# Kernel optimization log

Hardware: AMD Instinct MI355X
Metric: run time of the kernel (lower is better)

Reference implementation:

```python
import jax, jax.numpy as jnp
import numpy as np

RF = 16       # receptive_field
STRIDE = 16   # sim_strides
ALPHA = 0.3   # tf.keras LeakyReLU default alpha
EPS = 1e-3    # tf.keras BatchNormalization default epsilon


def _leaky(x):
    return jnp.where(x > 0, x, ALPHA * x)


def _bn_train(x, gamma, beta):
    # training-mode batch norm over (B, H, W), channel-last
    mu = jnp.mean(x, axis=(0, 1, 2))
    var = jnp.var(x, axis=(0, 1, 2))
    return (x - mu) * jax.lax.rsqrt(var + EPS) * gamma + beta


def _cbl(x, W, gamma, beta):
    # 1x1 conv (== channel matmul) + BN + LeakyReLU
    y = jnp.einsum('bhwc,cd->bhwd', x, W)
    return _leaky(_bn_train(y, gamma, beta))


def setup_inputs() -> dict:
    key = jax.random.key(0)
    ks = jax.random.split(key, 4)
    B, H, Wd, C = 4, 64, 64, 256
    s = 1.0 / np.sqrt(C)
    return {
        'inputs': jax.random.normal(ks[0], (B, H, Wd, C), jnp.float32),
        'Wq': jax.random.normal(ks[1], (C, C), jnp.float32) * s,
        'gq': jnp.ones((C,), jnp.float32), 'bq': jnp.zeros((C,), jnp.float32),
        'Wk': jax.random.normal(ks[2], (C, C), jnp.float32) * s,
        'gk': jnp.ones((C,), jnp.float32), 'bk': jnp.zeros((C,), jnp.float32),
        'Wv': jax.random.normal(ks[3], (C, C), jnp.float32) * s,
        'gv': jnp.ones((C,), jnp.float32), 'bv': jnp.zeros((C,), jnp.float32),
        'g1': jnp.ones((C,), jnp.float32), 'b1': jnp.zeros((C,), jnp.float32),
    }


def _windows(x):
    # x: [B,H,W,C] -> [B, nH*nW, RF, RF, C] overlapping-capable window gather
    H, Wd = x.shape[1], x.shape[2]
    nH = (H - RF) // STRIDE + 1
    nW = (Wd - RF) // STRIDE + 1
    ih = (jnp.arange(nH) * STRIDE)[:, None] + jnp.arange(RF)[None, :]  # [nH,RF]
    iw = (jnp.arange(nW) * STRIDE)[:, None] + jnp.arange(RF)[None, :]  # [nW,RF]
    xw = x[:, ih][:, :, :, iw]            # [B,nH,RF,nW,RF,C]
    xw = xw.transpose(0, 1, 3, 2, 4, 5)   # [B,nH,nW,RF,RF,C]
    return xw.reshape(x.shape[0], nH * nW, RF, RF, x.shape[3])


def reference(inputs, Wq, gq, bq, Wk, gk, bk, Wv, gv, bv, g1, b1):
    Q = _cbl(inputs, Wq, gq, bq)   # [B,H,W,C]
    K = _cbl(inputs, Wk, gk, bk)
    V = _cbl(inputs, Wv, gv, bv)
    C = Q.shape[-1]
    Kw = _windows(K)               # [B,N,RF,RF,C]
    Vw = _windows(V)
    # full-Q x window-K attention, summed over windows (matches nested loop)
    scores = jnp.einsum('bijc,bnpqc->bnijpq', Q, Kw) / jnp.sqrt(jnp.asarray(C, Q.dtype))
    scores = _leaky(scores)
    yout = jnp.einsum('bnijpq,bnpqc->bijc', scores, Vw)  # sum over windows n
    y = _bn_train(yout, g1, b1)
    # softmax jointly over spatial axes (1,2)
    m = jnp.max(y, axis=(1, 2), keepdims=True)
    e = jnp.exp(y - m)
    return e / jnp.sum(e, axis=(1, 2), keepdims=True)
```

## Files before the change

### kernel.cpp

```cpp
#include <hip/hip_runtime.h>
#include <stdint.h>


typedef __attribute__((ext_vector_type(8)))  short short8;
typedef __attribute__((ext_vector_type(4)))  float f32x4;
typedef __attribute__((ext_vector_type(16))) float f32x16;
typedef __attribute__((ext_vector_type(4)))  unsigned short ushort4v;

#define ALPHA 0.3f
#define EPS   1e-3
#define NTOT  16384.0

__device__ __forceinline__ unsigned short f2bf(float f){
  unsigned u = __float_as_uint(f);
  u += 0x7FFFu + ((u>>16)&1u);
  return (unsigned short)(u>>16);
}
__device__ __forceinline__ float bf2f(unsigned short u){
  return __uint_as_float((unsigned)u << 16);
}
__device__ __forceinline__ float lrelu(float x){ return fmaxf(x, ALPHA*x); }

__global__ __launch_bounds__(256)
void k_prep(const float* __restrict__ X,
            const float* __restrict__ Wq,
            const float* __restrict__ Wk,
            const float* __restrict__ Wv,
            unsigned short* __restrict__ Xb,
            unsigned short* __restrict__ Wt,
            float* __restrict__ zws){
  int blk = blockIdx.x, tid = threadIdx.x;
  if (blk < 4096){
    int i = (blk*256 + tid)*4;
    float4 v = *(const float4*)(X + i);
    ushort4v o; o.x = f2bf(v.x); o.y = f2bf(v.y); o.z = f2bf(v.z); o.w = f2bf(v.w);
    *(ushort4v*)(Xb + i) = o;
  } else {
    int o = (blk - 4096)*256 + tid;
    int p = o >> 16, rem = o & 65535;
    int j = rem >> 8, c = rem & 255;
    const float* W = (p==0) ? Wq : ((p==1) ? Wk : Wv);
    Wt[o] = f2bf(W[c*256 + j]);
    if (o < 5120) zws[o] = 0.f;
  }
}

__global__ __launch_bounds__(256)
void k_qkv_gemm(const unsigned short* __restrict__ X,
                const unsigned short* __restrict__ Wt,
                unsigned short* __restrict__ YQK, unsigned short* __restrict__ Yv,
                double* __restrict__ st){
  __shared__ __align__(16) unsigned short At[64*264];
  __shared__ __align__(16) unsigned short Bt[64*264];
  int tid = threadIdx.x;
  int g = blockIdx.x;
  int xcd = g & 7, r = g >> 3;
  int nb = r % 12, mb = xcd*32 + r/12;
#pragma unroll
  for (int it = 0; it < 8; ++it){
    int s = it*256 + tid;
    int row = s >> 5, ch = s & 31;
    uint4 a = *(const uint4*)(X  + ((size_t)(mb*64 + row))*256 + ch*8);
    uint4 b = *(const uint4*)(Wt + ((size_t)(nb*64 + row))*256 + ch*8);
    *(uint4*)(At + row*264 + ch*8) = a;
    *(uint4*)(Bt + row*264 + ch*8) = b;
  }
  __syncthreads();
  int lane = tid & 63, wv = tid >> 6;
  int ln15 = lane & 15, quad = lane >> 4;
  int rw = (wv & 1)*32, cw = (wv >> 1)*32;
  f32x4 acc[2][2] = {};
#pragma unroll
  for (int ks = 0; ks < 8; ++ks){
    short8 afr[2], bfr[2];
#pragma unroll
    for (int mt = 0; mt < 2; ++mt){
      int rr = rw + mt*16 + ln15;
      afr[mt] = *(const short8*)(At + rr*264 + (ks*4+quad)*8);
    }
#pragma unroll
    for (int nt = 0; nt < 2; ++nt){
      int rr = cw + nt*16 + ln15;
      bfr[nt] = *(const short8*)(Bt + rr*264 + (ks*4+quad)*8);
    }
#pragma unroll
    for (int mt = 0; mt < 2; ++mt)
#pragma unroll
      for (int nt = 0; nt < 2; ++nt)
        acc[mt][nt] = __builtin_amdgcn_mfma_f32_16x16x32_bf16(afr[mt], bfr[nt], acc[mt][nt], 0,0,0);
  }
  float ps[2] = {0.f, 0.f}, pq[2] = {0.f, 0.f};
#pragma unroll
  for (int mt = 0; mt < 2; ++mt)
#pragma unroll
    for (int nt = 0; nt < 2; ++nt)
#pragma unroll
      for (int rr = 0; rr < 4; ++rr){
        float v = acc[mt][nt][rr];
        ps[nt] += v; pq[nt] += v*v;
      }
  if (nb < 8){
    int proj = nb >> 2;
    unsigned short* base = YQK + (size_t)proj*(16384*256);
    int l5c = ln15 >> 3, j = ln15 & 7;
#pragma unroll
    for (int mt = 0; mt < 2; ++mt){
      int gg = (mb*64 + rw + mt*16) >> 5;
      int l31r0 = ((rw + mt*16) & 31) + quad*4;
#pragma unroll
      for (int nt = 0; nt < 2; ++nt){
        int ks2 = ((nb & 3)*64 + cw + nt*16) >> 4;
#pragma unroll
        for (int rr = 0; rr < 4; ++rr){
          size_t chunk = (size_t)((gg*16 + ks2)*64 + l5c*32 + l31r0 + rr);
          base[chunk*8 + j] = f2bf(acc[mt][nt][rr]);
        }
      }
    }
  } else {
    int vc0 = (nb - 8)*64 + cw;
#pragma unroll
    for (int mt = 0; mt < 2; ++mt)
#pragma unroll
      for (int nt = 0; nt < 2; ++nt)
#pragma unroll
        for (int rr = 0; rr < 4; ++rr){
          int row = mb*64 + rw + mt*16 + quad*4 + rr;
          Yv[(size_t)row*256 + vc0 + nt*16 + ln15] = f2bf(acc[mt][nt][rr]);
        }
  }
  __syncthreads();
  float* red = (float*)At;
  if (tid < 128) red[tid] = 0.f;
  __syncthreads();
#pragma unroll
  for (int nt = 0; nt < 2; ++nt){
    int colL = cw + nt*16 + ln15;
    atomicAdd(&red[colL],      ps[nt]);
    atomicAdd(&red[64 + colL], pq[nt]);
  }
  __syncthreads();
  if (tid < 64){
    int cc = nb*64 + tid;
    atomicAdd(&st[cc],       (double)red[tid]);
    atomicAdd(&st[768 + cc], (double)red[64 + tid]);
  }
}

__global__ __launch_bounds__(256)
void k_bn(const unsigned short* __restrict__ YQK, const unsigned short* __restrict__ Yv,
          const double* __restrict__ st,
          const float* __restrict__ gq, const float* __restrict__ bq,
          const float* __restrict__ gk, const float* __restrict__ bk,
          const float* __restrict__ gv, const float* __restrict__ bv,
          unsigned short* __restrict__ Qf, unsigned short* __restrict__ Kf,
          unsigned short* __restrict__ Vf){
  __shared__ float sc_s[256], sh_s[256];
  __shared__ unsigned short tile[64][66];
  int tid = threadIdx.x;
  int blk = blockIdx.x;
  if (blk < 4096){
    int proj = blk >> 11;
    {
      int c = tid;
      int cc = proj*256 + c;
      double mu  = st[cc]     * (1.0/NTOT);
      double var = st[768+cc] * (1.0/NTOT) - mu*mu;
      double g = proj ? (double)gk[c] : (double)gq[c];
      double b = proj ? (double)bk[c] : (double)bq[c];
      double a = g / sqrt(var + EPS);
      float f = proj ? 1.f : 0.0625f;
      sc_s[c] = (float)a * f;
      sh_s[c] = (float)(b - mu*a) * f;
    }
    __syncthreads();
    int oc = blk*256 + tid;
    int rest = oc & 524287;
    int ks = (rest >> 6) & 15, l5c = (rest >> 5) & 1;
    int ch0 = ks*16 + l5c*8;
    uint4 yin = *(const uint4*)(YQK + (size_t)oc*8);
    const unsigned short* yp = (const unsigned short*)&yin;
    const float* sc = sc_s + ch0;
    const float* sh = sh_s + ch0;
    unsigned short rr[8];
#pragma unroll
    for (int e = 0; e < 8; ++e){
      float v = bf2f(yp[e]);
      rr[e] = f2bf(lrelu(v*sc[e] + sh[e]));
    }
    uint4 u;
    u.x = (unsigned)rr[0] | ((unsigned)rr[1]<<16);
    u.y = (unsigned)rr[2] | ((unsigned)rr[3]<<16);
    u.z = (unsigned)rr[4] | ((unsigned)rr[5]<<16);
    u.w = (unsigned)rr[6] | ((unsigned)rr[7]<<16);
    *(uint4*)((proj ? Kf : Qf) + (size_t)rest*8) = u;
  } else {
    int b2 = blk - 4096;
    int pt = b2 & 63, ct = (b2 >> 6) & 3, b = b2 >> 8;
    if (tid < 64){
      int c = ct*64 + tid;
      int cc = 512 + c;
      double mu  = st[cc]     * (1.0/NTOT);
      double var = st[768+cc] * (1.0/NTOT) - mu*mu;
      double a = (double)gv[c] / sqrt(var + EPS);
      sc_s[tid] = (float)a;
      sh_s[tid] = (float)((double)bv[c] - mu*a);
    }
    __syncthreads();
#pragma unroll
    for (int kpass = 0; kpass < 2; ++kpass){
      int idx = kpass*256 + tid;
      int px = idx >> 3, co = idx & 7;
      size_t t = (size_t)b*4096 + pt*64 + px;
      uint4 u = *(const uint4*)(Yv + t*256 + ct*64 + co*8);
      const unsigned short* up = (const unsigned short*)&u;
      int c0 = co*8;
#pragma unroll
      for (int e = 0; e < 8; ++e){
        float v = bf2f(up[e]);
        tile[px][c0+e] = f2bf(lrelu(v*sc_s[c0+e] + sh_s[c0+e]));
      }
    }
    __syncthreads();
#pragma unroll
    for (int it = 0; it < 2; ++it){
      int m = it*256 + tid;
      int c2 = m >> 3, kg = m & 7;
      int ch = ct*64 + c2;
      int gc = b*8 + (ch >> 5), l31c = ch & 31;
      int kp = pt*4 + (kg >> 1), l5k = kg & 1;
      unsigned short r0 = tile[kg*8+0][c2], r1 = tile[kg*8+1][c2];
      unsigned short r2 = tile[kg*8+2][c2], r3 = tile[kg*8+3][c2];
      unsigned short r4 = tile[kg*8+4][c2], r5 = tile[kg*8+5][c2];
      unsigned short r6 = tile[kg*8+6][c2], r7 = tile[kg*8+7][c2];
      uint4 u;
      u.x = (unsigned)r0 | ((unsigned)r1<<16);
      u.y = (unsigned)r2 | ((unsigned)r3<<16);
      u.z = (unsigned)r4 | ((unsigned)r5<<16);
      u.w = (unsigned)r6 | ((unsigned)r7<<16);
      *(uint4*)(Vf + ((size_t)((gc*256 + kp)*64 + l5k*32 + l31c))*8) = u;
    }
  }
}

__global__ __launch_bounds__(512, 4)
void k_attn(const unsigned short* __restrict__ Qf,
            const unsigned short* __restrict__ Kf,
            const unsigned short* __restrict__ Vf,
            float* __restrict__ P0, float* __restrict__ P1){
  __shared__ __align__(16) unsigned short Ql[64*256];
  __shared__ __align__(16) unsigned short Sl[64*264];
  int tid = threadIdx.x;
  int blk = blockIdx.x;
  int qt = blk >> 3, combo = blk & 7;
  int b = combo >> 1, half = combo & 1;
  int q0 = qt*64;
  int lane = tid & 63, w = tid >> 6;
  int l31 = lane & 31, l5 = lane >> 5;
  float* P = half ? P1 : P0;

  int gq0 = b*128 + qt*2;
  {
    const uint4* src = (const uint4*)(Qf + (size_t)gq0*8192);
    uint4* dst = (uint4*)Ql;
#pragma unroll
    for (int it = 0; it < 4; ++it) dst[it*512 + tid] = src[it*512 + tid];
  }
  __syncthreads();

  f32x16 acc2[2] = {};
  int gk0 = b*128 + half*64 + w;
  const unsigned short* kb = Kf + (size_t)gk0*8192 + lane*8;
  const unsigned short* vb = Vf + ((size_t)((b*8 + w)*256 + half*128))*512 + lane*8;
  const unsigned short* qa0 = Ql + lane*8;
  const unsigned short* qa1 = Ql + 16*512 + lane*8;

  for (int kt = 0; kt < 8; ++kt){
    f32x16 a1[2] = {};
    const unsigned short* kbt = kb + (size_t)kt*8*8192;
    __builtin_amdgcn_s_setprio(1);
#pragma unroll
    for (int ks = 0; ks < 16; ++ks){
      short8 kf = *(const short8*)(kbt + ks*512);
      short8 q0v = *(const short8*)(qa0 + ks*512);
      short8 q1v = *(const short8*)(qa1 + ks*512);
      a1[0] = __builtin_amdgcn_mfma_f32_32x32x16_bf16(q0v, kf, a1[0], 0, 0, 0);
      a1[1] = __builtin_amdgcn_mfma_f32_32x32x16_bf16(q1v, kf, a1[1], 0, 0, 0);
    }
    __builtin_amdgcn_s_setprio(0);
    __syncthreads();
#pragma unroll
    for (int reg = 0; reg < 16; ++reg){
      int rloc = (reg & 3) + 8*(reg >> 2) + 4*l5;
      float x0 = a1[0][reg], x1 = a1[1][reg];
      Sl[rloc*264 + w*32 + l31]        = f2bf(fmaxf(x0, 0.3f*x0));
      Sl[(32 + rloc)*264 + w*32 + l31] = f2bf(fmaxf(x1, 0.3f*x1));
    }
    __syncthreads();
    const unsigned short* vbt = vb + (size_t)kt*16*512;
    __builtin_amdgcn_s_setprio(1);
#pragma unroll
    for (int kk = 0; kk < 16; ++kk){
      short8 vf = *(const short8*)(vbt + kk*512);
      short8 s0 = *(const short8*)(Sl + (     l31)*264 + kk*16 + l5*8);
      short8 s1 = *(const short8*)(Sl + (32 + l31)*264 + kk*16 + l5*8);
      acc2[0] = __builtin_amdgcn_mfma_f32_32x32x16_bf16(s0, vf, acc2[0], 0, 0, 0);
      acc2[1] = __builtin_amdgcn_mfma_f32_32x32x16_bf16(s1, vf, acc2[1], 0, 0, 0);
    }
    __builtin_amdgcn_s_setprio(0);
  }
#pragma unroll
  for (int c = 0; c < 2; ++c)
#pragma unroll
    for (int reg = 0; reg < 16; ++reg){
      int row = q0 + c*32 + (reg & 3) + 8*(reg >> 2) + 4*l5;
      P[((size_t)b*4096 + row)*256 + w*32 + l31] = acc2[c][reg];
    }
}

__global__ __launch_bounds__(256)
void k_red(const float* __restrict__ P0, const float* __restrict__ P1,
           float* __restrict__ yout, double* __restrict__ st){
  __shared__ float redS[4][256];
  __shared__ float redQ[4][256];
  int tid = threadIdx.x;
  int cg = (tid & 63)*4, pg = tid >> 6;
  int r0 = blockIdx.x*32;
  float s0=0,s1=0,s2=0,s3=0,q0=0,q1=0,q2=0,q3=0;
#pragma unroll
  for (int k = 0; k < 8; ++k){
    size_t idx = (size_t)(r0 + pg + k*4)*256 + cg;
    float4 a = *(const float4*)(P0 + idx);
    float4 b = *(const float4*)(P1 + idx);
    float4 v; v.x=a.x+b.x; v.y=a.y+b.y; v.z=a.z+b.z; v.w=a.w+b.w;
    *(float4*)(yout + idx) = v;
    s0 += v.x; q0 += v.x*v.x;
    s1 += v.y; q1 += v.y*v.y;
    s2 += v.z; q2 += v.z*v.z;
    s3 += v.w; q3 += v.w*v.w;
  }
  *(float4*)(&redS[pg][cg]) = make_float4(s0,s1,s2,s3);
  *(float4*)(&redQ[pg][cg]) = make_float4(q0,q1,q2,q3);
  __syncthreads();
  float s = redS[0][tid] + redS[1][tid] + redS[2][tid] + redS[3][tid];
  float q = redQ[0][tid] + redQ[1][tid] + redQ[2][tid] + redQ[3][tid];
  atomicAdd(&st[1536 + tid], (double)s);
  atomicAdd(&st[1792 + tid], (double)q);
}

__global__ __launch_bounds__(256)
void k_soft1(const float* __restrict__ yout, const double* __restrict__ st,
             const float* __restrict__ g1, float* __restrict__ sums){
  __shared__ float redL[16][64];
  __shared__ float sA[64], sK[64];
  int tid = threadIdx.x;
  int chunk = blockIdx.x, ct = blockIdx.y, b = blockIdx.z;
  int cg = (tid & 15)*4, pg = tid >> 4;
  if (tid < 64){
    int cc = ct*64 + tid;
    double mu  = st[1536 + cc]*(1.0/NTOT);
    double var = st[1792 + cc]*(1.0/NTOT) - mu*mu;
    double a = g1[cc] / sqrt(var + EPS);
    sA[tid] = (float)a;
    sK[tid] = (float)(a*mu);
  }
  __syncthreads();
  float a0=sA[cg], a1=sA[cg+1], a2=sA[cg+2], a3=sA[cg+3];
  float K0=sK[cg], K1=sK[cg+1], K2=sK[cg+2], K3=sK[cg+3];
  const float* base = yout + ((size_t)b*4096 + chunk*256)*256 + ct*64 + cg;
  float s0=0,s1=0,s2=0,s3=0;
#pragma unroll
  for (int k = 0; k < 16; ++k){
    float4 v = *(const float4*)(base + (size_t)(pg + k*16)*256);
    s0 += __expf(v.x*a0 - K0);
    s1 += __expf(v.y*a1 - K1);
    s2 += __expf(v.z*a2 - K2);
    s3 += __expf(v.w*a3 - K3);
  }
  *(float4*)(&redL[pg][cg]) = make_float4(s0,s1,s2,s3);
  __syncthreads();
  if (tid < 64){
    float tot = 0.f;
#pragma unroll
    for (int p = 0; p < 16; ++p) tot += redL[p][tid];
    atomicAdd(&sums[b*256 + ct*64 + tid], tot);
  }
}

__global__ __launch_bounds__(256)
void k_soft2(const float* __restrict__ yout, const double* __restrict__ st,
             const float* __restrict__ g1, const float* __restrict__ sums,
             float* __restrict__ out){
  __shared__ float sA[64], sK[64], sR[64];
  int tid = threadIdx.x;
  int chunk = blockIdx.x, ct = blockIdx.y, b = blockIdx.z;
  int cg = (tid & 15)*4, pg = tid >> 4;
  if (tid < 64){
    int cc = ct*64 + tid;
    double mu  = st[1536 + cc]*(1.0/NTOT);
    double var = st[1792 + cc]*(1.0/NTOT) - mu*mu;
    double a = g1[cc] / sqrt(var + EPS);
    sA[tid] = (float)a;
    sK[tid] = (float)(a*mu);
    sR[tid] = 1.f / sums[b*256 + cc];
  }
  __syncthreads();
  float a0=sA[cg], a1=sA[cg+1], a2=sA[cg+2], a3=sA[cg+3];
  float K0=sK[cg], K1=sK[cg+1], K2=sK[cg+2], K3=sK[cg+3];
  float r0=sR[cg], r1=sR[cg+1], r2=sR[cg+2], r3=sR[cg+3];
  const float* base = yout + ((size_t)b*4096 + chunk*256)*256 + ct*64 + cg;
  float* obase = out + ((size_t)b*4096 + chunk*256)*256 + ct*64 + cg;
#pragma unroll
  for (int k = 0; k < 16; ++k){
    size_t off = (size_t)(pg + k*16)*256;
    float4 v = *(const float4*)(base + off);
    float4 o;
    o.x = __expf(v.x*a0 - K0) * r0;
    o.y = __expf(v.y*a1 - K1) * r1;
    o.z = __expf(v.z*a2 - K2) * r2;
    o.w = __expf(v.w*a3 - K3) * r3;
    *(float4*)(obase + off) = o;
  }
}

extern "C" void kernel_launch(void* const* d_in, const int* in_sizes, int n_in,
                              void* d_out, int out_size, void* d_ws, size_t ws_size,
                              hipStream_t stream){
  (void)in_sizes; (void)n_in; (void)out_size; (void)ws_size;
  const float* X  = (const float*)d_in[0];
  const float* Wq = (const float*)d_in[1];
  const float* gq = (const float*)d_in[2];
  const float* bq = (const float*)d_in[3];
  const float* Wk = (const float*)d_in[4];
  const float* gk = (const float*)d_in[5];
  const float* bk = (const float*)d_in[6];
  const float* Wv = (const float*)d_in[7];
  const float* gv = (const float*)d_in[8];
  const float* bv = (const float*)d_in[9];
  const float* g1 = (const float*)d_in[10];

  char* ws = (char*)d_ws;
  double*         st   = (double*)ws;
  float*          sums = (float*)(ws + 16384);
  unsigned short* Wt   = (unsigned short*)(ws + 26624);
  unsigned short* Xb   = (unsigned short*)(ws + 419840);
  unsigned short* YQK  = (unsigned short*)(ws + 8808448);
  unsigned short* Yv   = (unsigned short*)(ws + 25585664);
  unsigned short* Kf   = (unsigned short*)(ws + 33974272);
  unsigned short* Vf   = (unsigned short*)(ws + 42362880);
  float*          P1   = (float*)(ws + 50751488);
  unsigned short* Qf   = Xb;
  float*          P0   = (float*)(ws + 8808448);
  float*          yo   = (float*)(ws + 33974272);

  k_prep    <<<4864, 256, 0, stream>>>(X, Wq, Wk, Wv, Xb, Wt, (float*)st);
  k_qkv_gemm<<<3072, 256, 0, stream>>>(Xb, Wt, YQK, Yv, st);
  k_bn      <<<5120, 256, 0, stream>>>(YQK, Yv, st, gq, bq, gk, bk, gv, bv, Qf, Kf, Vf);
  k_attn    <<<512, 512, 0, stream>>>(Qf, Kf, Vf, P0, P1);
  k_red     <<<512, 256, 0, stream>>>(P0, P1, yo, st);
  k_soft1   <<<dim3(16,4,4), 256, 0, stream>>>(yo, st, g1, sums);
  k_soft2   <<<dim3(16,4,4), 256, 0, stream>>>(yo, st, g1, sums, (float*)d_out);
}
```

Measured before the change: 241.0 us.

## Enlarge QKV GEMM tiles to 128x128 with direct global-to-LDS K-chunk loads

The QKV projection GEMM now uses 128x128 output tiles per block, with each wave computing 64x64, instead of 64x64 tiles. The K dimension is streamed in 64-wide chunks using global_load_lds, which writes straight into shared memory, rather than staging the full K=256 slab through registers. The grid shrinks from 3072 to 768 blocks. Larger tiles raise operand reuse per load and cut redundant global reads, at the cost of fewer blocks, unpadded LDS rows that may cause bank conflicts, and an unpipelined load/compute loop with two barriers per chunk.

```diff
diff --git a/kernel.cpp b/kernel.cpp
--- a/kernel.cpp
+++ b/kernel.cpp
@@ -10,6 +10,10 @@
 #define ALPHA 0.3f
 #define EPS   1e-3
 #define NTOT  16384.0
+
+#define GLOAD_LDS16(gp, lp) __builtin_amdgcn_global_load_lds( \
+    (const __attribute__((address_space(1))) void*)(gp), \
+    (__attribute__((address_space(3))) void*)(lp), 16, 0, 0)
 
 __device__ __forceinline__ unsigned short f2bf(float f){
   unsigned u = __float_as_uint(f);
@@ -50,100 +54,102 @@
                 const unsigned short* __restrict__ Wt,
                 unsigned short* __restrict__ YQK, unsigned short* __restrict__ Yv,
                 double* __restrict__ st){
-  __shared__ __align__(16) unsigned short At[64*264];
-  __shared__ __align__(16) unsigned short Bt[64*264];
+  __shared__ __align__(16) unsigned short At[128*64];
+  __shared__ __align__(16) unsigned short Bt[128*64];
   int tid = threadIdx.x;
   int g = blockIdx.x;
-  int xcd = g & 7, r = g >> 3;
-  int nb = r % 12, mb = xcd*32 + r/12;
-#pragma unroll
-  for (int it = 0; it < 8; ++it){
-    int s = it*256 + tid;
-    int row = s >> 5, ch = s & 31;
-    uint4 a = *(const uint4*)(X  + ((size_t)(mb*64 + row))*256 + ch*8);
-    uint4 b = *(const uint4*)(Wt + ((size_t)(nb*64 + row))*256 + ch*8);
-    *(uint4*)(At + row*264 + ch*8) = a;
-    *(uint4*)(Bt + row*264 + ch*8) = b;
-  }
-  __syncthreads();
-  int lane = tid & 63, wv = tid >> 6;
+  int xcd = g & 7, r8 = g >> 3;
+  int mb = xcd*16 + r8/6, nb = r8 % 6;
+  int lane = tid & 63, w = tid >> 6;
   int ln15 = lane & 15, quad = lane >> 4;
-  int rw = (wv & 1)*32, cw = (wv >> 1)*32;
-  f32x4 acc[2][2] = {};
-#pragma unroll
-  for (int ks = 0; ks < 8; ++ks){
-    short8 afr[2], bfr[2];
-#pragma unroll
-    for (int mt = 0; mt < 2; ++mt){
-      int rr = rw + mt*16 + ln15;
-      afr[mt] = *(const short8*)(At + rr*264 + (ks*4+quad)*8);
-    }
-#pragma unroll
-    for (int nt = 0; nt < 2; ++nt){
-      int rr = cw + nt*16 + ln15;
-      bfr[nt] = *(const short8*)(Bt + rr*264 + (ks*4+quad)*8);
-    }
-#pragma unroll
-    for (int mt = 0; mt < 2; ++mt)
-#pragma unroll
-      for (int nt = 0; nt < 2; ++nt)
-        acc[mt][nt] = __builtin_amdgcn_mfma_f32_16x16x32_bf16(afr[mt], bfr[nt], acc[mt][nt], 0,0,0);
-  }
-  float ps[2] = {0.f, 0.f}, pq[2] = {0.f, 0.f};
-#pragma unroll
-  for (int mt = 0; mt < 2; ++mt)
-#pragma unroll
-    for (int nt = 0; nt < 2; ++nt)
+  int rw = (w & 1)*64, cw = (w >> 1)*64;
+
+  const unsigned short* gaL = X  + ((size_t)(mb*128 + (lane>>3)))*256 + (lane&7)*8;
+  const unsigned short* gbL = Wt + ((size_t)(nb*128 + (lane>>3)))*256 + (lane&7)*8;
+
+  f32x4 acc[4][4] = {};
+  for (int kt = 0; kt < 4; ++kt){
+    const unsigned short* ga = gaL + kt*64;
+    const unsigned short* gb = gbL + kt*64;
+#pragma unroll
+    for (int j = 0; j < 4; ++j){
+      int s = w*4 + j;
+      GLOAD_LDS16(ga + (size_t)s*8*256, At + s*512);
+      GLOAD_LDS16(gb + (size_t)s*8*256, Bt + s*512);
+    }
+    __syncthreads();
+#pragma unroll
+    for (int ksub = 0; ksub < 2; ++ksub){
+      short8 af[4], bf[4];
+#pragma unroll
+      for (int mt = 0; mt < 4; ++mt)
+        af[mt] = *(const short8*)(At + (rw + mt*16 + ln15)*64 + ksub*32 + quad*8);
+#pragma unroll
+      for (int nt = 0; nt < 4; ++nt)
+        bf[nt] = *(const short8*)(Bt + (cw + nt*16 + ln15)*64 + ksub*32 + quad*8);
+#pragma unroll
+      for (int mt = 0; mt < 4; ++mt)
+#pragma unroll
+        for (int nt = 0; nt < 4; ++nt)
+          acc[mt][nt] = __builtin_amdgcn_mfma_f32_16x16x32_bf16(af[mt], bf[nt], acc[mt][nt], 0,0,0);
+    }
+    __syncthreads();
+  }
+  float ps[4] = {0,0,0,0}, pq[4] = {0,0,0,0};
+#pragma unroll
+  for (int mt = 0; mt < 4; ++mt)
+#pragma unroll
+    for (int nt = 0; nt < 4; ++nt)
 #pragma unroll
       for (int rr = 0; rr < 4; ++rr){
         float v = acc[mt][nt][rr];
         ps[nt] += v; pq[nt] += v*v;
       }
-  if (nb < 8){
-    int proj = nb >> 2;
+  if (nb < 4){
+    int proj = nb >> 1;
     unsigned short* base = YQK + (size_t)proj*(16384*256);
-    int l5c = ln15 >> 3, j = ln15 & 7;
-#pragma unroll
-    for (int mt = 0; mt < 2; ++mt){
-      int gg = (mb*64 + rw + mt*16) >> 5;
-      int l31r0 = ((rw + mt*16) & 31) + quad*4;
-#pragma unroll
-      for (int nt = 0; nt < 2; ++nt){
-        int ks2 = ((nb & 3)*64 + cw + nt*16) >> 4;
+#pragma unroll
+    for (int nt = 0; nt < 4; ++nt){
+      int ch_g = (nb&1)*128 + cw + nt*16 + ln15;
+      int ksf = ch_g >> 4, l5c = (ch_g >> 3) & 1, j = ch_g & 7;
+#pragma unroll
+      for (int mt = 0; mt < 4; ++mt){
+        int row0 = mb*128 + rw + mt*16 + quad*4;
+        int gg = row0 >> 5, l31r0 = row0 & 31;
 #pragma unroll
         for (int rr = 0; rr < 4; ++rr){
-          size_t chunk = (size_t)((gg*16 + ks2)*64 + l5c*32 + l31r0 + rr);
+          size_t chunk = (size_t)((gg*16 + ksf)*64 + l5c*32 + l31r0 + rr);
           base[chunk*8 + j] = f2bf(acc[mt][nt][rr]);
         }
       }
     }
   } else {
-    int vc0 = (nb - 8)*64 + cw;
-#pragma unroll
-    for (int mt = 0; mt < 2; ++mt)
-#pragma unroll
-      for (int nt = 0; nt < 2; ++nt)
+    int vc0 = (nb - 4)*128 + cw;
+#pragma unroll
+    for (int mt = 0; mt < 4; ++mt)
+#pragma unroll
+      for (int nt = 0; nt < 4; ++nt)
 #pragma unroll
         for (int rr = 0; rr < 4; ++rr){
-          int row = mb*64 + rw + mt*16 + quad*4 + rr;
+          int row = mb*128 + rw + mt*16 + quad*4 + rr;
           Yv[(size_t)row*256 + vc0 + nt*16 + ln15] = f2bf(acc[mt][nt][rr]);
         }
   }
   __syncthreads();
   float* red = (float*)At;
-  if (tid < 128) red[tid] = 0.f;
-  __syncthreads();
-#pragma unroll
-  for (int nt = 0; nt < 2; ++nt){
+  red[tid] = 0.f;
+  __syncthreads();
+#pragma unroll
+  for (int nt = 0; nt < 4; ++nt){
     int colL = cw + nt*16 + ln15;
-    atomicAdd(&red[colL],      ps[nt]);
-    atomicAdd(&red[64 + colL], pq[nt]);
-  }
-  __syncthreads();
-  if (tid < 64){
-    int cc = nb*64 + tid;
+    atomicAdd(&red[colL],       ps[nt]);
+    atomicAdd(&red[128 + colL], pq[nt]);
+  }
+  __syncthreads();
+  if (tid < 128){
+    int cc = nb*128 + tid;
     atomicAdd(&st[cc],       (double)red[tid]);
-    atomicAdd(&st[768 + cc], (double)red[64 + tid]);
+    atomicAdd(&st[768 + cc], (double)red[128 + tid]);
   }
 }
 
@@ -454,7 +460,7 @@
   float*          yo   = (float*)(ws + 33974272);
 
   k_prep    <<<4864, 256, 0, stream>>>(X, Wq, Wk, Wv, Xb, Wt, (float*)st);
-  k_qkv_gemm<<<3072, 256, 0, stream>>>(Xb, Wt, YQK, Yv, st);
+  k_qkv_gemm<<<768, 256, 0, stream>>>(Xb, Wt, YQK, Yv, st);
   k_bn      <<<5120, 256, 0, stream>>>(YQK, Yv, st, gq, bq, gk, bk, gv, bv, Qf, Kf, Vf);
   k_attn    <<<512, 512, 0, stream>>>(Qf, Kf, Vf, P0, P1);
   k_red     <<<512, 256, 0, stream>>>(P0, P1, yo, st);
```

Result: faster. 230.0 us (-4.5%).
